# Kernel optimization log

Measured on AMD Instinct MI355X. Metric: run time of the kernel, lower is better.

Reference implementation:

```python
import jax, jax.numpy as jnp
import numpy as np

B = 131072   # number of graphs (ranked lists)
G = 128      # candidates per graph
TEMPERATURE = 1.0

def setup_inputs() -> dict:
    key = jax.random.key(0)
    k1, k2 = jax.random.split(key)
    scores = jax.random.normal(k1, (B * G,), dtype=jnp.float32)
    labels = jax.random.randint(k2, (B * G,), 0, 2, dtype=jnp.int32)  # binary relevance
    batch = jnp.repeat(jnp.arange(B, dtype=jnp.int32), G)             # segment ids, sorted
    return {"scores": scores, "labels": labels, "batch": batch}

def reference(scores, labels, batch):
    # batch encodes B contiguous equal-size segments of length G; reshape replaces
    # the original per-graph Python loop with one vectorized pass.
    s = scores.reshape(B, G) / TEMPERATURE            # [B, G]
    l = labels.reshape(B, G).astype(s.dtype)          # [B, G]
    probs = jax.nn.softmax(s, axis=1)
    pos = jnp.arange(1, G + 1, dtype=s.dtype)
    disc = 1.0 / jnp.log2(pos + 1.0)                  # [G]
    expected_dcg = jnp.sum(probs * l * disc, axis=1)  # [B]
    sorted_l = -jnp.sort(-l, axis=1)                  # descending sort of labels
    idcg = jnp.sum(sorted_l * disc, axis=1)           # [B]
    valid = idcg > 0                                  # graphs with labels.sum()==0 contribute loss 0
    ndcg = expected_dcg / jnp.where(valid, idcg, 1.0)
    loss_g = jnp.where(valid, 1.0 - ndcg, 0.0)
    # original counts every non-NaN graph, including zero-label graphs -> divide by B
    return jnp.sum(loss_g) / B
```

## Files before the change

kernel.cpp:

```cpp
#include <hip/hip_runtime.h>
#include <math.h>


#define G 128

__global__ void build_tables_kernel(float* __restrict__ tabs) {
    int t = threadIdx.x;
    if (t < G) {
        tabs[t] = 1.0f / log2f((float)(t + 2));
    }
    if (t <= G) {
        float s = 0.0f;
        for (int p = 1; p <= t; ++p) s += 1.0f / log2f((float)(p + 1));
        tabs[G + t] = s;
    }
}

__global__ __launch_bounds__(256) void ndcg_main_kernel(
        const float* __restrict__ scores,
        const int*   __restrict__ labels,
        const float* __restrict__ tabs,
        float*       __restrict__ partials,
        int B) {
    const int t = threadIdx.x;

    __shared__ float cum_s[G + 1];
    if (t <= G) cum_s[t] = tabs[G + t];
    __syncthreads();

    const int g = blockIdx.x * 256 + t;
    float loss = 0.0f;
    if (g < B) {
        const float4* sp = (const float4*)(scores + (long long)g * G);
        const int4*   lp = (const int4*)(labels + (long long)g * G);

        float4 s[8];
        int4   l[8];
#pragma unroll
        for (int i = 0; i < 8; ++i) s[i] = sp[i];
#pragma unroll
        for (int i = 0; i < 8; ++i) l[i] = lp[i];

        const float4* dv = (const float4*)tabs;

        float es0 = 0.f, es1 = 0.f, es2 = 0.f, es3 = 0.f;
        float nu0 = 0.f, nu1 = 0.f, nu2 = 0.f, nu3 = 0.f;
        int cnt = 0;
#pragma unroll
        for (int i = 0; i < 8; ++i) {
            const float4 d = dv[i];
            const float e0 = __expf(s[i].x);
            const float e1 = __expf(s[i].y);
            const float e2 = __expf(s[i].z);
            const float e3 = __expf(s[i].w);
            es0 += e0; es1 += e1; es2 += e2; es3 += e3;
            nu0 += e0 * (l[i].x ? d.x : 0.0f);
            nu1 += e1 * (l[i].y ? d.y : 0.0f);
            nu2 += e2 * (l[i].z ? d.z : 0.0f);
            nu3 += e3 * (l[i].w ? d.w : 0.0f);
            cnt += l[i].x + l[i].y + l[i].z + l[i].w;
        }
        const float esum = (es0 + es1) + (es2 + es3);
        const float num  = (nu0 + nu1) + (nu2 + nu3);
        const float idcg = cum_s[cnt];
        loss = (cnt > 0) ? (1.0f - num / (esum * idcg)) : 0.0f;
    }

    __shared__ float red[256];
    red[t] = loss;
    __syncthreads();
    for (int s2 = 128; s2 > 0; s2 >>= 1) {
        if (t < s2) red[t] += red[t + s2];
        __syncthreads();
    }
    if (t == 0) partials[blockIdx.x] = red[0];
}

__global__ void finalize_kernel(const float* __restrict__ partials, int n,
                                float* __restrict__ out, float invB) {
    __shared__ float red[256];
    float a = 0.0f;
    for (int i = threadIdx.x; i < n; i += 256) a += partials[i];
    red[threadIdx.x] = a;
    __syncthreads();
    for (int s = 128; s > 0; s >>= 1) {
        if (threadIdx.x < s) red[threadIdx.x] += red[threadIdx.x + s];
        __syncthreads();
    }
    if (threadIdx.x == 0) out[0] = red[0] * invB;
}

extern "C" void kernel_launch(void* const* d_in, const int* in_sizes, int n_in,
                              void* d_out, int out_size, void* d_ws, size_t ws_size,
                              hipStream_t stream) {
    const float* scores = (const float*)d_in[0];
    const int*   labels = (const int*)d_in[1];

    const int n = in_sizes[0];
    const int B = n / G;
    const int NB = (B + 255) / 256;

    float* tabs     = (float*)d_ws;
    float* partials = tabs + 512;

    build_tables_kernel<<<1, 256, 0, stream>>>(tabs);
    ndcg_main_kernel<<<NB, 256, 0, stream>>>(scores, labels, tabs, partials, B);
    finalize_kernel<<<1, 256, 0, stream>>>(partials, NB, (float*)d_out,
                                           1.0f / (float)B);
}
```

Before: 168.6 us.

## Map each graph to 16 lanes for coalesced loads and shuffle reductions

Before, each thread read one whole 512-byte graph, so neighbouring threads hit addresses 512 bytes apart. Now each 64-lane wave handles 16 graphs, with 16 lanes per graph reading adjacent float4s, so global loads coalesce. Per-graph sums are combined with xor shuffles inside each 16-lane group. Per-block totals are gathered with a shared-memory atomicAdd instead of a tree reduction. The trade-off is extra shuffle instructions and a float summation order that is no longer fixed, so results may vary slightly between runs.

```diff
diff --git a/kernel.cpp b/kernel.cpp
--- a/kernel.cpp
+++ b/kernel.cpp
@@ -16,64 +16,81 @@
     }
 }
 
-__global__ __launch_bounds__(256) void ndcg_main_kernel(
+__global__ __launch_bounds__(256, 4) void ndcg_main_kernel(
         const float* __restrict__ scores,
         const int*   __restrict__ labels,
         const float* __restrict__ tabs,
         float*       __restrict__ partials,
         int B) {
-    const int t = threadIdx.x;
+    const int t    = threadIdx.x;
+    const int lane = t & 63;
+    const int li   = lane & 15;
+    const int gs   = lane >> 4;
+    const int wib  = t >> 6;
+    const long long wave  = (long long)blockIdx.x * 4 + wib;
+    const long long gbase = wave * 16;
 
-    __shared__ float cum_s[G + 1];
-    if (t <= G) cum_s[t] = tabs[G + t];
+    __shared__ float bsum;
+    if (t == 0) bsum = 0.0f;
     __syncthreads();
 
-    const int g = blockIdx.x * 256 + t;
-    float loss = 0.0f;
-    if (g < B) {
-        const float4* sp = (const float4*)(scores + (long long)g * G);
-        const int4*   lp = (const int4*)(labels + (long long)g * G);
+    if (gbase < B) {
+        const float4* dv = (const float4*)tabs;
+        const float4 dA = dv[li];
+        const float4 dB = dv[16 + li];
 
-        float4 s[8];
-        int4   l[8];
+        float4 sA[4], sB[4];
+        int4   lA[4], lB[4];
 #pragma unroll
-        for (int i = 0; i < 8; ++i) s[i] = sp[i];
+        for (int q = 0; q < 4; ++q) {
+            const long long g = gbase + q * 4 + gs;
+            const float4* sp = (const float4*)(scores + g * G);
+            const int4*   lp = (const int4*)(labels + g * G);
+            sA[q] = sp[li];
+            sB[q] = sp[16 + li];
+            lA[q] = lp[li];
+            lB[q] = lp[16 + li];
+        }
+
+        float esum[4], num[4], cntf[4];
 #pragma unroll
-        for (int i = 0; i < 8; ++i) l[i] = lp[i];
+        for (int q = 0; q < 4; ++q) {
+            float e0 = __expf(sA[q].x), e1 = __expf(sA[q].y);
+            float e2 = __expf(sA[q].z), e3 = __expf(sA[q].w);
+            float e4 = __expf(sB[q].x), e5 = __expf(sB[q].y);
+            float e6 = __expf(sB[q].z), e7 = __expf(sB[q].w);
+            esum[q] = ((e0 + e1) + (e2 + e3)) + ((e4 + e5) + (e6 + e7));
+            num[q]  = ((e0 * (lA[q].x ? dA.x : 0.f) + e1 * (lA[q].y ? dA.y : 0.f))
+                     + (e2 * (lA[q].z ? dA.z : 0.f) + e3 * (lA[q].w ? dA.w : 0.f)))
+                    + ((e4 * (lB[q].x ? dB.x : 0.f) + e5 * (lB[q].y ? dB.y : 0.f))
+                     + (e6 * (lB[q].z ? dB.z : 0.f) + e7 * (lB[q].w ? dB.w : 0.f)));
+            cntf[q] = (float)((lA[q].x + lA[q].y + lA[q].z + lA[q].w)
+                            + (lB[q].x + lB[q].y + lB[q].z + lB[q].w));
+        }
 
-        const float4* dv = (const float4*)tabs;
+#pragma unroll
+        for (int m = 1; m <= 8; m <<= 1) {
+#pragma unroll
+            for (int q = 0; q < 4; ++q) {
+                esum[q] += __shfl_xor(esum[q], m, 64);
+                num[q]  += __shfl_xor(num[q],  m, 64);
+                cntf[q] += __shfl_xor(cntf[q], m, 64);
+            }
+        }
 
-        float es0 = 0.f, es1 = 0.f, es2 = 0.f, es3 = 0.f;
-        float nu0 = 0.f, nu1 = 0.f, nu2 = 0.f, nu3 = 0.f;
-        int cnt = 0;
+        if (li == 0) {
+            float acc = 0.0f;
 #pragma unroll
-        for (int i = 0; i < 8; ++i) {
-            const float4 d = dv[i];
-            const float e0 = __expf(s[i].x);
-            const float e1 = __expf(s[i].y);
-            const float e2 = __expf(s[i].z);
-            const float e3 = __expf(s[i].w);
-            es0 += e0; es1 += e1; es2 += e2; es3 += e3;
-            nu0 += e0 * (l[i].x ? d.x : 0.0f);
-            nu1 += e1 * (l[i].y ? d.y : 0.0f);
-            nu2 += e2 * (l[i].z ? d.z : 0.0f);
-            nu3 += e3 * (l[i].w ? d.w : 0.0f);
-            cnt += l[i].x + l[i].y + l[i].z + l[i].w;
+            for (int q = 0; q < 4; ++q) {
+                const int c = (int)cntf[q];
+                const float idcg = tabs[G + c];
+                acc += (c > 0) ? (1.0f - num[q] / (esum[q] * idcg)) : 0.0f;
+            }
+            atomicAdd(&bsum, acc);
         }
-        const float esum = (es0 + es1) + (es2 + es3);
-        const float num  = (nu0 + nu1) + (nu2 + nu3);
-        const float idcg = cum_s[cnt];
-        loss = (cnt > 0) ? (1.0f - num / (esum * idcg)) : 0.0f;
     }
-
-    __shared__ float red[256];
-    red[t] = loss;
     __syncthreads();
-    for (int s2 = 128; s2 > 0; s2 >>= 1) {
-        if (t < s2) red[t] += red[t + s2];
-        __syncthreads();
-    }
-    if (t == 0) partials[blockIdx.x] = red[0];
+    if (t == 0) partials[blockIdx.x] = bsum;
 }
 
 __global__ void finalize_kernel(const float* __restrict__ partials, int n,
@@ -98,7 +115,7 @@
 
     const int n = in_sizes[0];
     const int B = n / G;
-    const int NB = (B + 255) / 256;
+    const int NB = (B + 15) / 16 / 4;
 
     float* tabs     = (float*)d_ws;
     float* partials = tabs + 512;
```

New measurement: 195.5 us. +16.0%, slower.
